# Performance work log

Hardware: AMD Instinct MI355X
Metric: run time of the kernel (lower is better)

## Reference

```python
import jax, jax.numpy as jnp
import numpy as np

B, C, T = 32, 64, 2048
H = 1024
LEAK = 0.9
SPECTRAL_RADIUS = 0.9
INPUT_SCALE = 1.0


def setup_inputs() -> dict:
    key = jax.random.key(0)
    k_x, k_win, k_wres = jax.random.split(key, 3)
    x = jax.random.normal(k_x, (B, C, T), dtype=jnp.float32)
    W_in = jax.random.normal(k_win, (H, C), dtype=jnp.float32) * INPUT_SCALE
    W_res = jax.random.normal(k_wres, (H, H), dtype=jnp.float32)
    # normalize to target spectral radius (via largest singular value, as in reset_parameters)
    s0 = jnp.linalg.norm(W_res, ord=2)
    W_res = W_res * (SPECTRAL_RADIUS / s0)
    b = jnp.zeros((H,), dtype=jnp.float32)
    return {"x": x, "W_in": W_in, "W_res": W_res, "b": b}


def reference(x, W_in, W_res, b):
    # x: (B, C, T) -> states: (B, H, T)
    # Precompute input projection for all timesteps: (B, T, H)
    x_proj = jnp.einsum('bct,hc->bth', x, W_in) + b
    h0 = jnp.zeros((x.shape[0], W_res.shape[0]), dtype=x.dtype)

    def step(h, xp_t):  # xp_t: (B, H)
        pre = jnp.tanh(xp_t + h @ W_res.T)
        h_new = (1.0 - LEAK) * h + LEAK * pre
        return h_new, h_new

    # scan over time: xs shape (T, B, H)
    _, states = jax.lax.scan(step, h0, jnp.swapaxes(x_proj, 0, 1))
    # (T, B, H) -> (B, H, T)
    return jnp.transpose(states, (1, 2, 0))
```

## Files before the change

kernel.cpp:

```cpp
#include <hip/hip_runtime.h>
#include <math.h>

#define B_  32
#define C_  64
#define T_  2048
#define H_  1024

#define NGROUP 16
#define BPG    2
#define NSLICE 16
#define ROWS   64
#define NWG    (NGROUP * NSLICE)
#define NTHR   512
#define CHUNK  68


__global__ void esn_init_kernel(unsigned* __restrict__ cnt,
                                float* __restrict__ hbuf) {
    int i = blockIdx.x * blockDim.x + threadIdx.x;
    if (i < 1024) cnt[i] = 0u;
    hbuf[i] = 0.0f;
}

__global__ __launch_bounds__(256) void esn_xproj_kernel(
        const float* __restrict__ x,
        const float* __restrict__ W_in,
        const float* __restrict__ bias,
        float* __restrict__ out) {
    __shared__ float xs[32 * 256];
    const int tid = threadIdx.x;
    const int t0  = blockIdx.x * 256;
    const int h0  = blockIdx.y * 8;
    const int b   = blockIdx.z;
    const float* xb = x + (size_t)b * C_ * T_ + t0;

    float acc[8];
#pragma unroll
    for (int h = 0; h < 8; ++h) acc[h] = 0.0f;

    for (int ch = 0; ch < 2; ++ch) {
        for (int idx = tid; idx < 32 * 64; idx += 256) {
            const int c  = idx >> 6;
            const int t4 = idx & 63;
            float4 v = *(const float4*)(xb + (size_t)(ch * 32 + c) * T_ + t4 * 4);
            *(float4*)(&xs[c * 256 + t4 * 4]) = v;
        }
        __syncthreads();
        for (int c = 0; c < 32; ++c) {
            const float xv = xs[c * 256 + tid];
#pragma unroll
            for (int h = 0; h < 8; ++h)
                acc[h] = fmaf(xv, W_in[(size_t)(h0 + h) * C_ + ch * 32 + c], acc[h]);
        }
        __syncthreads();
    }

    float* ob = out + (size_t)b * H_ * T_ + t0 + tid;
#pragma unroll
    for (int h = 0; h < 8; ++h)
        ob[(size_t)(h0 + h) * T_] = acc[h] + bias[h0 + h];
}

__global__ __launch_bounds__(NTHR, 2) void esn_recur_kernel(
        const float* W_res,
        float* out,
        unsigned* cnt,
        float* hbuf) {
    const int wg   = blockIdx.x;
    const int g    = wg >> 4;
    const int s    = wg & 15;
    const int tid  = threadIdx.x;
    const int wave = tid >> 6;
    const int lane = tid & 63;
    const int cg   = lane & 15;
    const int rt   = (wave << 2) + (lane >> 4);
    const int row0 = s * ROWS + rt * 2;
    const int b0   = g * BPG;

    unsigned long long* hb64 = (unsigned long long*)hbuf;

    float4 w0[16], w1[16];
    {
        const float4* p0 = (const float4*)(W_res + (size_t)row0 * H_) + (cg << 4);
        const float4* p1 = (const float4*)(W_res + (size_t)(row0 + 1) * H_) + (cg << 4);
#pragma unroll
        for (int k = 0; k < 16; ++k) { w0[k] = p0[k]; w1[k] = p1[k]; }
    }

    __shared__ __align__(16) float hl[BPG][16 * CHUNK];

    const int fb = tid >> 8;
    const int fc = (tid << 2) & 1023;
    float* hlw = &hl[fb][(fc >> 6) * CHUNK + (fc & 63)];

    const bool fin  = (cg < BPG);
    const int  fbat = cg;
    float* op0 = out + ((size_t)(b0 + (fin ? fbat : 0)) * H_ + row0) * (size_t)T_;
    float* op1 = op0 + T_;

    float xp0 = fin ? op0[0] : 0.0f;
    float xp1 = fin ? op1[0] : 0.0f;

    unsigned long long sink = 0ull;
    unsigned* grpcnt = &cnt[g * 32];

    for (int t = 0; t < T_; ++t) {
        const int p = t & 1;

        {
            const size_t i64 = (((size_t)p * B_ + b0 + fb) * H_ + fc) >> 1;
            unsigned long long q0 = __hip_atomic_fetch_add(
                hb64 + i64, 0ull, __ATOMIC_RELAXED, __HIP_MEMORY_SCOPE_AGENT);
            unsigned long long q1 = __hip_atomic_fetch_add(
                hb64 + i64 + 1, 0ull, __ATOMIC_RELAXED, __HIP_MEMORY_SCOPE_AGENT);
            float4 v = make_float4(__uint_as_float((unsigned)q0),
                                   __uint_as_float((unsigned)(q0 >> 32)),
                                   __uint_as_float((unsigned)q1),
                                   __uint_as_float((unsigned)(q1 >> 32)));
            *(float4*)hlw = v;
        }
        __syncthreads();
        __builtin_amdgcn_sched_barrier(0);

        float xp0n = 0.0f, xp1n = 0.0f;
        if (fin && t + 1 < T_) { xp0n = op0[t + 1]; xp1n = op1[t + 1]; }

        float s00 = 0.f, s01 = 0.f, s10 = 0.f, s11 = 0.f;
        const float* h0 = &hl[0][cg * CHUNK];
        const float* h1 = &hl[1][cg * CHUNK];
#pragma unroll
        for (int k = 0; k < 16; ++k) {
            const float4 ha  = *(const float4*)(h0 + 4 * k);
            const float4 hb4 = *(const float4*)(h1 + 4 * k);
            const float4 u = w0[k], v = w1[k];
            s00 = fmaf(u.x, ha.x, s00);  s00 = fmaf(u.y, ha.y, s00);
            s00 = fmaf(u.z, ha.z, s00);  s00 = fmaf(u.w, ha.w, s00);
            s10 = fmaf(v.x, ha.x, s10);  s10 = fmaf(v.y, ha.y, s10);
            s10 = fmaf(v.z, ha.z, s10);  s10 = fmaf(v.w, ha.w, s10);
            s01 = fmaf(u.x, hb4.x, s01); s01 = fmaf(u.y, hb4.y, s01);
            s01 = fmaf(u.z, hb4.z, s01); s01 = fmaf(u.w, hb4.w, s01);
            s11 = fmaf(v.x, hb4.x, s11); s11 = fmaf(v.y, hb4.y, s11);
            s11 = fmaf(v.z, hb4.z, s11); s11 = fmaf(v.w, hb4.w, s11);
        }
#pragma unroll
        for (int m = 1; m <= 8; m <<= 1) {
            s00 += __shfl_xor(s00, m);
            s01 += __shfl_xor(s01, m);
            s10 += __shfl_xor(s10, m);
            s11 += __shfl_xor(s11, m);
        }

        if (fin) {
            const float sA = fbat ? s01 : s00;
            const float sB = fbat ? s11 : s10;
            const float pre0 = tanhf(xp0 + sA);
            const float pre1 = tanhf(xp1 + sB);
            const float* hc = &hl[fbat][((row0 >> 6) * CHUNK) + (row0 & 63)];
            const float hn0 = fmaf(0.1f, hc[0], 0.9f * pre0);
            const float hn1 = fmaf(0.1f, hc[1], 0.9f * pre1);
            op0[t] = hn0;
            op1[t] = hn1;
            const unsigned long long pack =
                ((unsigned long long)__float_as_uint(hn1) << 32) |
                (unsigned long long)__float_as_uint(hn0);
            const size_t w64 =
                (((size_t)((t + 1) & 1) * B_ + b0 + fbat) * H_ + row0) >> 1;
            sink ^= __hip_atomic_exchange(hb64 + w64, pack,
                                          __ATOMIC_RELAXED,
                                          __HIP_MEMORY_SCOPE_AGENT);
        }
        xp0 = xp0n;
        xp1 = xp1n;

        if (t + 1 < T_) {
            __syncthreads();
            __builtin_amdgcn_sched_barrier(0);
            if (tid == 0) {
                __hip_atomic_fetch_add(grpcnt, 1u, __ATOMIC_RELAXED,
                                       __HIP_MEMORY_SCOPE_AGENT);
                const unsigned tgt = (unsigned)NSLICE * (unsigned)(t + 1);
                while (__hip_atomic_fetch_add(grpcnt, 0u, __ATOMIC_RELAXED,
                                              __HIP_MEMORY_SCOPE_AGENT) < tgt) {
                    __builtin_amdgcn_s_sleep(1);
                }
            }
            __syncthreads();
            __builtin_amdgcn_sched_barrier(0);
        }
    }

    if (sink == 0x9E3779B97F4A7C15ull && tid == 0) cnt[512] = 1u;
}

extern "C" void kernel_launch(void* const* d_in, const int* in_sizes, int n_in,
                              void* d_out, int out_size, void* d_ws, size_t ws_size,
                              hipStream_t stream) {
    const float* x     = (const float*)d_in[0];
    const float* W_in  = (const float*)d_in[1];
    const float* W_res = (const float*)d_in[2];
    const float* bias  = (const float*)d_in[3];
    float* out = (float*)d_out;

    unsigned* cnt  = (unsigned*)d_ws;
    float*    hbuf = (float*)((char*)d_ws + 4096);

    esn_init_kernel<<<256, 256, 0, stream>>>(cnt, hbuf);

    dim3 g1(T_ / 256, H_ / 8, B_);
    esn_xproj_kernel<<<g1, 256, 0, stream>>>(x, W_in, bias, out);

    esn_recur_kernel<<<NWG, NTHR, 0, stream>>>(W_res, out, cnt, hbuf);
}
```

Before: 6.651 ms.

## Spread shared hidden-state buffer across cache lines and keep previous state in registers

Lays out the global hidden-state exchange buffer so that each 16-byte quad of state sits in its own 128-byte slot when the workspace is large enough. This is meant to cut cache-line contention between workgroups that do atomic reads and writes on neighbouring state entries. The leak term now uses a register copy of the previous hidden value instead of reading it back from LDS, and the LDS row padding changes from 68 to 66. In exchange the buffer uses eight times more memory, so the init kernel must zero a larger region.

```diff
diff --git a/kernel.cpp b/kernel.cpp
--- a/kernel.cpp
+++ b/kernel.cpp
@@ -12,14 +12,13 @@
 #define ROWS   64
 #define NWG    (NGROUP * NSLICE)
 #define NTHR   512
-#define CHUNK  68
-
-
-__global__ void esn_init_kernel(unsigned* __restrict__ cnt,
-                                float* __restrict__ hbuf) {
+#define CHUNK  66
+
+
+__global__ void esn_init_kernel(unsigned* cnt, unsigned* hbuf32, int n) {
     int i = blockIdx.x * blockDim.x + threadIdx.x;
     if (i < 1024) cnt[i] = 0u;
-    hbuf[i] = 0.0f;
+    if (i < n) hbuf32[i] = 0u;
 }
 
 __global__ __launch_bounds__(256) void esn_xproj_kernel(
@@ -61,6 +60,7 @@
         ob[(size_t)(h0 + h) * T_] = acc[h] + bias[h0 + h];
 }
 
+template <int QSH>
 __global__ __launch_bounds__(NTHR, 2) void esn_recur_kernel(
         const float* W_res,
         float* out,
@@ -100,15 +100,19 @@
 
     float xp0 = fin ? op0[0] : 0.0f;
     float xp1 = fin ? op1[0] : 0.0f;
+    float hprev0 = 0.0f, hprev1 = 0.0f;
 
     unsigned long long sink = 0ull;
     unsigned* grpcnt = &cnt[g * 32];
 
+    const size_t qw_bat = (size_t)(b0 + (fin ? fbat : 0)) * H_;
+
     for (int t = 0; t < T_; ++t) {
         const int p = t & 1;
 
         {
-            const size_t i64 = (((size_t)p * B_ + b0 + fb) * H_ + fc) >> 1;
+            const size_t q   = ((size_t)(p * B_ + b0 + fb) * H_ + fc) >> 2;
+            const size_t i64 = q << (QSH - 1);
             unsigned long long q0 = __hip_atomic_fetch_add(
                 hb64 + i64, 0ull, __ATOMIC_RELAXED, __HIP_MEMORY_SCOPE_AGENT);
             unsigned long long q1 = __hip_atomic_fetch_add(
@@ -155,17 +159,19 @@
             const float sB = fbat ? s11 : s10;
             const float pre0 = tanhf(xp0 + sA);
             const float pre1 = tanhf(xp1 + sB);
-            const float* hc = &hl[fbat][((row0 >> 6) * CHUNK) + (row0 & 63)];
-            const float hn0 = fmaf(0.1f, hc[0], 0.9f * pre0);
-            const float hn1 = fmaf(0.1f, hc[1], 0.9f * pre1);
+            const float hn0 = fmaf(0.1f, hprev0, 0.9f * pre0);
+            const float hn1 = fmaf(0.1f, hprev1, 0.9f * pre1);
+            hprev0 = hn0;
+            hprev1 = hn1;
             op0[t] = hn0;
             op1[t] = hn1;
             const unsigned long long pack =
                 ((unsigned long long)__float_as_uint(hn1) << 32) |
                 (unsigned long long)__float_as_uint(hn0);
-            const size_t w64 =
-                (((size_t)((t + 1) & 1) * B_ + b0 + fbat) * H_ + row0) >> 1;
-            sink ^= __hip_atomic_exchange(hb64 + w64, pack,
+            const size_t qw  = ((size_t)(((t + 1) & 1) * B_) * H_ + qw_bat
+                                + (row0 & ~3)) >> 2;
+            const size_t i64 = (qw << (QSH - 1)) + ((row0 >> 1) & 1);
+            sink ^= __hip_atomic_exchange(hb64 + i64, pack,
                                           __ATOMIC_RELAXED,
                                           __HIP_MEMORY_SCOPE_AGENT);
         }
@@ -204,10 +210,18 @@
     unsigned* cnt  = (unsigned*)d_ws;
     float*    hbuf = (float*)((char*)d_ws + 4096);
 
-    esn_init_kernel<<<256, 256, 0, stream>>>(cnt, hbuf);
+    const size_t quads = (size_t)2 * B_ * H_ / 4;
+    const size_t spread_bytes = 4096 + (quads << 5) * 4;
+    const bool spread = (ws_size >= spread_bytes);
+    const int  n32 = (int)(spread ? (quads << 5) : (quads << 2));
+
+    esn_init_kernel<<<(n32 + 255) / 256, 256, 0, stream>>>(cnt, (unsigned*)hbuf, n32);
 
     dim3 g1(T_ / 256, H_ / 8, B_);
     esn_xproj_kernel<<<g1, 256, 0, stream>>>(x, W_in, bias, out);
 
-    esn_recur_kernel<<<NWG, NTHR, 0, stream>>>(W_res, out, cnt, hbuf);
-}
+    if (spread)
+        esn_recur_kernel<5><<<NWG, NTHR, 0, stream>>>(W_res, out, cnt, hbuf);
+    else
+        esn_recur_kernel<2><<<NWG, NTHR, 0, stream>>>(W_res, out, cnt, hbuf);
+}
```

Result: slower. 21.08 ms (+217.0%).

## Remap workgroups so each group shares an XCC and use plain loads for polling

Applied to the files above, without the earlier changes.

Workgroup-to-group mapping is permuted so the 16 slices of a batch group are likely dispatched to the same XCC. At startup each workgroup reads its XCC id, and a group-wide check decides whether all slices share an XCC. When they do, hidden-state reads and counter polling use plain atomic loads in place of fetch_add RMW operations. The previous-h value is also kept in registers instead of being reread from LDS, and the LDS chunk padding changes. The main risk is that the fast path depends on cache coherence within one XCC and on the assumed round-robin dispatch order.

```diff
diff --git a/kernel.cpp b/kernel.cpp
--- a/kernel.cpp
+++ b/kernel.cpp
@@ -12,14 +12,13 @@
 #define ROWS   64
 #define NWG    (NGROUP * NSLICE)
 #define NTHR   512
-#define CHUNK  68
-
-
-__global__ void esn_init_kernel(unsigned* __restrict__ cnt,
-                                float* __restrict__ hbuf) {
+#define CHUNK  66
+
+
+__global__ void esn_init_kernel(unsigned* cnt, unsigned* hbuf32) {
     int i = blockIdx.x * blockDim.x + threadIdx.x;
     if (i < 1024) cnt[i] = 0u;
-    hbuf[i] = 0.0f;
+    hbuf32[i] = 0u;
 }
 
 __global__ __launch_bounds__(256) void esn_xproj_kernel(
@@ -67,8 +66,8 @@
         unsigned* cnt,
         float* hbuf) {
     const int wg   = blockIdx.x;
-    const int g    = wg >> 4;
-    const int s    = wg & 15;
+    const int g    = (wg & 7) | (((wg >> 7) & 1) << 3);
+    const int s    = (wg >> 3) & 15;
     const int tid  = threadIdx.x;
     const int wave = tid >> 6;
     const int lane = tid & 63;
@@ -78,6 +77,34 @@
     const int b0   = g * BPG;
 
     unsigned long long* hb64 = (unsigned long long*)hbuf;
+    unsigned* grpcnt = &cnt[g * 32];
+    unsigned sink32 = 0u;
+    unsigned long long sink = 0ull;
+
+    unsigned xcc;
+    asm volatile("s_getreg_b32 %0, hwreg(HW_REG_XCC_ID)" : "=s"(xcc));
+    xcc = (xcc & 15u) + 1u;
+    if (tid == 0)
+        sink32 ^= __hip_atomic_exchange(&cnt[512 + g * 16 + s], xcc,
+                                        __ATOMIC_RELAXED,
+                                        __HIP_MEMORY_SCOPE_AGENT);
+    __syncthreads();
+    if (tid == 0) {
+        __hip_atomic_fetch_add(&cnt[g * 32 + 8], 1u, __ATOMIC_RELAXED,
+                               __HIP_MEMORY_SCOPE_AGENT);
+        while (__hip_atomic_fetch_add(&cnt[g * 32 + 8], 0u, __ATOMIC_RELAXED,
+                                      __HIP_MEMORY_SCOPE_AGENT)
+               < (unsigned)NSLICE) {
+            __builtin_amdgcn_s_sleep(1);
+        }
+    }
+    __syncthreads();
+    unsigned vx = xcc;
+    if (tid < NSLICE)
+        vx = __hip_atomic_fetch_add(&cnt[512 + g * 16 + tid], 0u,
+                                    __ATOMIC_RELAXED,
+                                    __HIP_MEMORY_SCOPE_AGENT);
+    const bool fastp = (__syncthreads_and((int)(vx == xcc)) != 0);
 
     float4 w0[16], w1[16];
     {
@@ -100,19 +127,26 @@
 
     float xp0 = fin ? op0[0] : 0.0f;
     float xp1 = fin ? op1[0] : 0.0f;
-
-    unsigned long long sink = 0ull;
-    unsigned* grpcnt = &cnt[g * 32];
+    float hprev0 = 0.0f, hprev1 = 0.0f;
 
     for (int t = 0; t < T_; ++t) {
         const int p = t & 1;
 
         {
-            const size_t i64 = (((size_t)p * B_ + b0 + fb) * H_ + fc) >> 1;
-            unsigned long long q0 = __hip_atomic_fetch_add(
-                hb64 + i64, 0ull, __ATOMIC_RELAXED, __HIP_MEMORY_SCOPE_AGENT);
-            unsigned long long q1 = __hip_atomic_fetch_add(
-                hb64 + i64 + 1, 0ull, __ATOMIC_RELAXED, __HIP_MEMORY_SCOPE_AGENT);
+            const size_t i64 = (((size_t)(p * B_ + b0 + fb) * H_) + fc) >> 1;
+            unsigned long long q0, q1;
+            if (fastp) {
+                q0 = __hip_atomic_load(hb64 + i64, __ATOMIC_RELAXED,
+                                       __HIP_MEMORY_SCOPE_AGENT);
+                q1 = __hip_atomic_load(hb64 + i64 + 1, __ATOMIC_RELAXED,
+                                       __HIP_MEMORY_SCOPE_AGENT);
+            } else {
+                q0 = __hip_atomic_fetch_add(hb64 + i64, 0ull, __ATOMIC_RELAXED,
+                                            __HIP_MEMORY_SCOPE_AGENT);
+                q1 = __hip_atomic_fetch_add(hb64 + i64 + 1, 0ull,
+                                            __ATOMIC_RELAXED,
+                                            __HIP_MEMORY_SCOPE_AGENT);
+            }
             float4 v = make_float4(__uint_as_float((unsigned)q0),
                                    __uint_as_float((unsigned)(q0 >> 32)),
                                    __uint_as_float((unsigned)q1),
@@ -155,16 +189,17 @@
             const float sB = fbat ? s11 : s10;
             const float pre0 = tanhf(xp0 + sA);
             const float pre1 = tanhf(xp1 + sB);
-            const float* hc = &hl[fbat][((row0 >> 6) * CHUNK) + (row0 & 63)];
-            const float hn0 = fmaf(0.1f, hc[0], 0.9f * pre0);
-            const float hn1 = fmaf(0.1f, hc[1], 0.9f * pre1);
+            const float hn0 = fmaf(0.1f, hprev0, 0.9f * pre0);
+            const float hn1 = fmaf(0.1f, hprev1, 0.9f * pre1);
+            hprev0 = hn0;
+            hprev1 = hn1;
             op0[t] = hn0;
             op1[t] = hn1;
             const unsigned long long pack =
                 ((unsigned long long)__float_as_uint(hn1) << 32) |
                 (unsigned long long)__float_as_uint(hn0);
             const size_t w64 =
-                (((size_t)((t + 1) & 1) * B_ + b0 + fbat) * H_ + row0) >> 1;
+                (((size_t)(((t + 1) & 1) * B_ + b0 + fbat) * H_) + row0) >> 1;
             sink ^= __hip_atomic_exchange(hb64 + w64, pack,
                                           __ATOMIC_RELAXED,
                                           __HIP_MEMORY_SCOPE_AGENT);
@@ -179,8 +214,15 @@
                 __hip_atomic_fetch_add(grpcnt, 1u, __ATOMIC_RELAXED,
                                        __HIP_MEMORY_SCOPE_AGENT);
                 const unsigned tgt = (unsigned)NSLICE * (unsigned)(t + 1);
-                while (__hip_atomic_fetch_add(grpcnt, 0u, __ATOMIC_RELAXED,
-                                              __HIP_MEMORY_SCOPE_AGENT) < tgt) {
+                for (;;) {
+                    unsigned c;
+                    if (fastp)
+                        c = __hip_atomic_load(grpcnt, __ATOMIC_RELAXED,
+                                              __HIP_MEMORY_SCOPE_AGENT);
+                    else
+                        c = __hip_atomic_fetch_add(grpcnt, 0u, __ATOMIC_RELAXED,
+                                                   __HIP_MEMORY_SCOPE_AGENT);
+                    if (c >= tgt) break;
                     __builtin_amdgcn_s_sleep(1);
                 }
             }
@@ -189,7 +231,8 @@
         }
     }
 
-    if (sink == 0x9E3779B97F4A7C15ull && tid == 0) cnt[512] = 1u;
+    if (((sink ^ (unsigned long long)sink32) == 0x9E3779B97F4A7C15ull) && tid == 0)
+        cnt[1000] = 1u;
 }
 
 extern "C" void kernel_launch(void* const* d_in, const int* in_sizes, int n_in,
@@ -204,7 +247,7 @@
     unsigned* cnt  = (unsigned*)d_ws;
     float*    hbuf = (float*)((char*)d_ws + 4096);
 
-    esn_init_kernel<<<256, 256, 0, stream>>>(cnt, hbuf);
+    esn_init_kernel<<<256, 256, 0, stream>>>(cnt, (unsigned*)hbuf);
 
     dim3 g1(T_ / 256, H_ / 8, B_);
     esn_xproj_kernel<<<g1, 256, 0, stream>>>(x, W_in, bias, out);
```

Measured after the change: 18.59 ms. 179% more time.
